# Kernel optimization log

Hardware: AMD Instinct MI355X
Metric: run time of the kernel (lower is better)

## Reference

```python
import jax, jax.numpy as jnp
import numpy as np

B, S, D = 1, 2048, 2048
H, KVH, HD = 32, 8, 64
FFN = 8192
N_EXPERTS, TOP_K = 32, 4
EPS = 1e-5
NEG = -1e9


def setup_inputs() -> dict:
    key = jax.random.key(0)
    ks = jax.random.split(key, 24)
    s = 0.02
    inp = {}
    inp['hidden_states'] = jax.random.normal(ks[0], (B, S, D), jnp.float32)
    # RoPE tables: cos/sin of shape [B, S, HD]
    inv_freq = 1.0 / (10000.0 ** (np.arange(0, HD, 2, dtype=np.float32) / HD))
    t = np.arange(S, dtype=np.float32)
    freqs = np.outer(t, inv_freq)                      # [S, HD/2]
    emb = np.concatenate([freqs, freqs], axis=-1)      # [S, HD]
    inp['cos'] = jnp.asarray(np.cos(emb))[None].repeat(B, axis=0)
    inp['sin'] = jnp.asarray(np.sin(emb))[None].repeat(B, axis=0)
    # additive causal mask [B, 1, S, S]
    causal = jnp.where(jnp.tril(jnp.ones((S, S), bool)), 0.0, NEG).astype(jnp.float32)
    inp['attention_mask'] = jnp.broadcast_to(causal[None, None], (B, 1, S, S))
    # attention params
    inp['wq'] = jax.random.normal(ks[1], (H * HD, D), jnp.float32) * s
    inp['bq'] = jnp.zeros((H * HD,), jnp.float32)
    inp['wk'] = jax.random.normal(ks[2], (KVH * HD, D), jnp.float32) * s
    inp['bk'] = jnp.zeros((KVH * HD,), jnp.float32)
    inp['wv'] = jax.random.normal(ks[3], (KVH * HD, D), jnp.float32) * s
    inp['bv'] = jnp.zeros((KVH * HD,), jnp.float32)
    inp['wo'] = jax.random.normal(ks[4], (D, H * HD), jnp.float32) * s
    inp['bo'] = jnp.zeros((D,), jnp.float32)
    # norms
    inp['ln1_w'] = jnp.ones((D,), jnp.float32)
    inp['ln2_w'] = jnp.ones((D,), jnp.float32)
    # MoE gate + shared expert MLP
    inp['gate_w'] = jax.random.normal(ks[5], (N_EXPERTS, D), jnp.float32) * s
    inp['gate_b'] = jnp.zeros((N_EXPERTS,), jnp.float32)
    inp['w1'] = jax.random.normal(ks[6], (FFN, D), jnp.float32) * s
    inp['b1'] = jnp.zeros((FFN,), jnp.float32)
    inp['w2'] = jax.random.normal(ks[7], (D, FFN), jnp.float32) * s
    inp['b2'] = jnp.zeros((D,), jnp.float32)
    inp['w3'] = jax.random.normal(ks[8], (FFN, D), jnp.float32) * s
    inp['b3'] = jnp.zeros((FFN,), jnp.float32)
    return inp


def _rms_norm(x, w, eps=EPS):
    x32 = x.astype(jnp.float32)
    var = jnp.mean(x32 * x32, axis=-1, keepdims=True)
    return (w * (x32 * jax.lax.rsqrt(var + eps))).astype(x.dtype)


def _rotate_half(x):
    x1, x2 = jnp.split(x, 2, axis=-1)
    return jnp.concatenate([-x2, x1], axis=-1)


def _decoder_layer(hidden_states, cos, sin, attention_mask,
                   wq, bq, wk, bk, wv, bv, wo, bo, ln1_w, ln2_w,
                   gate_w, gate_b, w1, b1, w2, b2, w3, b3):
    residual = hidden_states
    x = _rms_norm(hidden_states, ln1_w)

    # projections -> [B, heads, S, HD]
    q = (x @ wq.T + bq).reshape(B, S, H, HD).transpose(0, 2, 1, 3)
    k = (x @ wk.T + bk).reshape(B, S, KVH, HD).transpose(0, 2, 1, 3)
    v = (x @ wv.T + bv).reshape(B, S, KVH, HD).transpose(0, 2, 1, 3)

    # RoPE (cos/sin unsqueezed on head dim)
    c, s_ = cos[:, None], sin[:, None]
    q = q * c + _rotate_half(q) * s_
    k = k * c + _rotate_half(k) * s_

    # GQA: repeat kv heads
    n_rep = H // KVH
    k = jnp.repeat(k, n_rep, axis=1)
    v = jnp.repeat(v, n_rep, axis=1)

    scaling = HD ** -0.5
    scores = jnp.einsum('bhqd,bhkd->bhqk', q, k) * scaling + attention_mask
    probs = jax.nn.softmax(scores.astype(jnp.float32), axis=-1).astype(q.dtype)
    attn = jnp.einsum('bhqk,bhkd->bhqd', probs, v)
    attn = attn.transpose(0, 2, 1, 3).reshape(B, S, H * HD)
    attn = attn @ wo.T + bo

    hidden_states = residual + attn
    residual = hidden_states
    x = _rms_norm(hidden_states, ln2_w)

    # MoE block (as written in source: router computed, but ALL tokens go
    # through one shared expert MLP; routing weights unused in output)
    flat = x.reshape(-1, D)
    router_logits = flat @ gate_w.T + gate_b                     # [B*S, E]
    rw = jax.nn.softmax(router_logits.astype(jnp.float32), axis=-1)
    rw_top, sel = jax.lax.top_k(rw, TOP_K)                       # computed, unused
    del rw_top, sel

    h1 = flat @ w1.T + b1
    h3 = flat @ w3.T + b3
    mlp = (jax.nn.silu(h1) * h3) @ w2.T + b2
    hidden_states = residual + mlp.reshape(B, S, D)
    return hidden_states


def reference(hidden_states, cos, sin, attention_mask,
              wq, bq, wk, bk, wv, bv, wo, bo, ln1_w, ln2_w,
              gate_w, gate_b, w1, b1, w2, b2, w3, b3):
    return _decoder_layer(hidden_states, cos, sin, attention_mask,
                          wq, bq, wk, bk, wv, bv, wo, bo, ln1_w, ln2_w,
                          gate_w, gate_b, w1, b1, w2, b2, w3, b3)
```

## Files before the change

kernel.cpp:

```cpp
#include <hip/hip_runtime.h>

#define S_LEN 2048
#define DMODEL 2048
#define NH 32
#define NKV 8
#define HD 64
#define FFN_DIM 8192

typedef __attribute__((ext_vector_type(4))) float f32x4;
typedef __attribute__((ext_vector_type(16))) float f32x16;
typedef __attribute__((ext_vector_type(8))) short bf16x8;

#define MFMA(a, b, c) __builtin_amdgcn_mfma_f32_16x16x32_bf16(a, b, c, 0, 0, 0)
#define MFMA32(a, b, c) __builtin_amdgcn_mfma_f32_32x32x16_bf16(a, b, c, 0, 0, 0)

__device__ __forceinline__ ushort f2bf(float f) {
  unsigned u = __float_as_uint(f);
  unsigned r = (u + 0x7fffu + ((u >> 16) & 1u)) >> 16;
  return (ushort)r;
}
__device__ __forceinline__ float bf2f(ushort s) {
  return __uint_as_float(((unsigned)s) << 16);
}
__device__ __forceinline__ unsigned cvtpk(float a, float b) {
  unsigned r;
  asm("v_cvt_pk_bf16_f32 %0, %1, %2" : "=v"(r) : "v"(a), "v"(b));
  return r;
}

__device__ __forceinline__ void gload16(const void* g, void* l) {
  __builtin_amdgcn_global_load_lds(
      (const __attribute__((address_space(1))) void*)g,
      (__attribute__((address_space(3))) void*)l, 16, 0, 0);
}

__global__ __launch_bounds__(256) void cvt_k(const float* __restrict__ in,
                                             ushort* __restrict__ out) {
  int i = blockIdx.x * 256 + threadIdx.x;
  f32x4 a = ((const f32x4*)in)[i * 2];
  f32x4 b = ((const f32x4*)in)[i * 2 + 1];
  bf16x8 r;
#pragma unroll
  for (int j = 0; j < 4; j++) r[j] = (short)f2bf(a[j]);
#pragma unroll
  for (int j = 0; j < 4; j++) r[4 + j] = (short)f2bf(b[j]);
  ((bf16x8*)out)[i] = r;
}

__global__ __launch_bounds__(256) void cvt_qkv_k(const float* __restrict__ wq,
                                                 const float* __restrict__ wk,
                                                 const float* __restrict__ wv,
                                                 ushort* __restrict__ dst) {
  int row = blockIdx.x;
  const float* src;
  if (row < 2048) src = wq + (size_t)row * DMODEL;
  else if (row < 2560) src = wk + (size_t)(row - 2048) * DMODEL;
  else src = wv + (size_t)(row - 2560) * DMODEL;
  int i = threadIdx.x * 8;
  f32x4 a = *(const f32x4*)(src + i);
  f32x4 b = *(const f32x4*)(src + i + 4);
  bf16x8 r;
#pragma unroll
  for (int j = 0; j < 4; j++) r[j] = (short)f2bf(a[j]);
#pragma unroll
  for (int j = 0; j < 4; j++) r[4 + j] = (short)f2bf(b[j]);
  *(bf16x8*)(dst + (size_t)row * DMODEL + i) = r;
}

__global__ __launch_bounds__(256) void cvt_w13_k(const float* __restrict__ w1,
                                                 const float* __restrict__ w3,
                                                 ushort* __restrict__ dst) {
  int r = blockIdx.x;
  int nb = r >> 8, i5 = r & 255;
  int wn = i5 >> 6, nf = (i5 >> 4) & 3, e = i5 & 15;
  int L = nb * 128 + wn * 32 + (nf >> 1) * 16 + e;
  const float* src = ((nf & 1) ? w3 : w1) + (size_t)L * DMODEL;
  int i = threadIdx.x * 8;
  f32x4 a = *(const f32x4*)(src + i);
  f32x4 b = *(const f32x4*)(src + i + 4);
  bf16x8 rr;
#pragma unroll
  for (int j = 0; j < 4; j++) rr[j] = (short)f2bf(a[j]);
#pragma unroll
  for (int j = 0; j < 4; j++) rr[4 + j] = (short)f2bf(b[j]);
  *(bf16x8*)(dst + (size_t)r * DMODEL + i) = rr;
}

__global__ __launch_bounds__(256) void bias3_k(const float* __restrict__ a,
                                               const float* __restrict__ b,
                                               const float* __restrict__ c,
                                               float* __restrict__ out) {
  int i = blockIdx.x * 256 + threadIdx.x;
  float v;
  if (i < 2048) v = a[i];
  else if (i < 2560) v = b[i - 2048];
  else v = c[i - 2560];
  out[i] = v;
}

__global__ __launch_bounds__(256) void rmsnorm_k(const float* __restrict__ in,
                                                 const float* __restrict__ w,
                                                 ushort* __restrict__ out) {
  const int row = blockIdx.x;
  const int tid = threadIdx.x;
  const float* x = in + (size_t)row * DMODEL;
  f32x4 v0 = *(const f32x4*)(x + tid * 8);
  f32x4 v1 = *(const f32x4*)(x + tid * 8 + 4);
  float ss = v0[0] * v0[0] + v0[1] * v0[1] + v0[2] * v0[2] + v0[3] * v0[3] +
             v1[0] * v1[0] + v1[1] * v1[1] + v1[2] * v1[2] + v1[3] * v1[3];
#pragma unroll
  for (int off = 32; off; off >>= 1) ss += __shfl_xor(ss, off, 64);
  __shared__ float red[4];
  if ((tid & 63) == 0) red[tid >> 6] = ss;
  __syncthreads();
  float tot = red[0] + red[1] + red[2] + red[3];
  float inv = rsqrtf(tot * (1.f / DMODEL) + 1e-5f);
#pragma unroll
  for (int i = 0; i < 8; i++) {
    int c = tid * 8 + i;
    float val = (i < 4) ? v0[i] : v1[i - 4];
    out[(size_t)row * DMODEL + c] = f2bf(w[c] * val * inv);
  }
}

enum { EPI_PART = 0, EPI_SILU2 = 1 };

#define QUAD(AS, BS, MROW, NCOL)                                     \
  _Pragma("unroll") for (int kk_ = 0; kk_ < 2; kk_++)                \
  _Pragma("unroll") for (int mf_ = 0; mf_ < 4; mf_++)                \
  _Pragma("unroll") for (int nf_ = 0; nf_ < 2; nf_++)                \
      acc[(MROW) + mf_][(NCOL) + nf_] =                              \
          MFMA(AS[2 * mf_ + kk_], BS[2 * nf_ + kk_],                 \
               acc[(MROW) + mf_][(NCOL) + nf_]);

#define PHASE_MID                                    \
  __builtin_amdgcn_sched_barrier(0);                 \
  __builtin_amdgcn_s_barrier();                      \
  asm volatile("s_waitcnt lgkmcnt(0)" ::: "memory"); \
  __builtin_amdgcn_sched_barrier(0);                 \
  __builtin_amdgcn_s_setprio(1);

#define PHASE_CLOSE                                  \
  __builtin_amdgcn_s_setprio(0);                     \
  __builtin_amdgcn_sched_barrier(0);                 \
  __builtin_amdgcn_s_barrier();

#define RD_A(PA0, PA1, J0)                           \
  _Pragma("unroll") for (int j_ = 0; j_ < 4; j_++) { \
    A_[2 * j_] = *(const bf16x8*)((PA0) + ((J0) + j_) * 1024);     \
    A_[2 * j_ + 1] = *(const bf16x8*)((PA1) + ((J0) + j_) * 1024); \
  }
#define RD_B(DST, PB0, PB1, J0)                      \
  _Pragma("unroll") for (int n_ = 0; n_ < 2; n_++) { \
    DST[2 * n_] = *(const bf16x8*)((PB0) + ((J0) + n_) * 1024);     \
    DST[2 * n_ + 1] = *(const bf16x8*)((PB1) + ((J0) + n_) * 1024); \
  }

template <int EPI>
__global__ __launch_bounds__(512, 2) void gemm256(
    const ushort* __restrict__ A, int lda, const ushort* __restrict__ B,
    int ldb, const float* __restrict__ b1v, const float* __restrict__ b3v,
    ushort* __restrict__ outb, int ldc, int K, int kspan, long long opart) {
  __shared__ __align__(16) ushort lds[65536];
  const int tid = threadIdx.x;
  const int l = tid & 63, w = tid >> 6;
  const int g = l >> 4, r16 = l & 15;
  const int wm = w >> 2, wn = w & 3;

  int nwg = gridDim.x * gridDim.y;
  int bid = blockIdx.y * gridDim.x + blockIdx.x;
  bid = (bid & 7) * (nwg >> 3) + (bid >> 3);
  const int m0 = (bid % gridDim.x) * 256;
  const int n0 = (bid / gridDim.x) * 256;
  const int z = blockIdx.z;

  const ushort* Ag = A + (size_t)z * kspan + (size_t)m0 * lda;
  const ushort* Bg = B + (size_t)z * kspan + (size_t)n0 * ldb;
  ushort* outbz = outb + (size_t)z * opart;

  const int NT = K >> 6, NI = NT >> 1;

  const int stgRow = w * 8 + (l >> 3);
  const int stgCol = ((l & 7) ^ (l >> 3)) * 8;

  const int xa = (r16 & 7) << 4;
  const int c0 = ((g * 16) ^ xa) >> 1;
  const int c1 = c0 ^ 32;
  const int aslot = wm ? 24576 : 8192;
  const int bslot = ((wn >> 1) ? 16384 : 0) + (wn & 1) * 4096;
  const ushort* pA0b0 = lds + aslot + r16 * 64 + c0;
  const ushort* pA1b0 = lds + aslot + r16 * 64 + c1;
  const ushort* pA0b1 = pA0b0 + 32768;
  const ushort* pA1b1 = pA1b0 + 32768;
  const ushort* pB0b0 = lds + bslot + r16 * 64 + c0;
  const ushort* pB1b0 = lds + bslot + r16 * 64 + c1;
  const ushort* pB0b1 = pB0b0 + 32768;
  const ushort* pB1b1 = pB1b0 + 32768;

  f32x4 acc[8][4];
#pragma unroll
  for (int i = 0; i < 8; i++)
#pragma unroll
    for (int j = 0; j < 4; j++) acc[i][j] = (f32x4){0, 0, 0, 0};

  auto stageA = [&](int slot, int tile, int hf) {
    ushort* dst = lds + ((tile & 1) * 32768 + slot * 8192 + w * 512);
    const ushort* src =
        Ag + (size_t)(hf * 128 + stgRow) * lda + tile * 64 + stgCol;
    gload16(src, dst);
    gload16(src + (size_t)64 * lda, dst + 4096);
  };
  auto stageB = [&](int slot, int tile, int hf) {
    ushort* dst = lds + ((tile & 1) * 32768 + slot * 8192 + w * 512);
    const ushort* src =
        Bg + (size_t)(hf * 128 + stgRow) * ldb + tile * 64 + stgCol;
    gload16(src, dst);
    gload16(src + (size_t)64 * ldb, dst + 4096);
  };

  stageB(0, 0, 0);
  stageB(2, 0, 1);
  stageA(1, 0, 0);
  stageA(3, 0, 1);
  stageB(0, 1, 0);
  stageB(2, 1, 1);
  asm volatile("s_waitcnt vmcnt(4)" ::: "memory");
  __builtin_amdgcn_s_barrier();

  bf16x8 A_[8], Blo[4], Bhi[4];

  for (int i = 0; i < NI; ++i) {
    const int ta = 2 * i, tb = 2 * i + 1;
    const bool st = (ta + 2 < NT);
    RD_A(pA0b0, pA1b0, 0);
    RD_B(Blo, pB0b0, pB1b0, 0);
    stageA(1, tb, 0);
    asm volatile("s_waitcnt lgkmcnt(8)" ::: "memory");
    PHASE_MID; QUAD(A_, Blo, 0, 0); PHASE_CLOSE;
    RD_B(Bhi, pB0b0, pB1b0, 2);
    stageA(3, tb, 1);
    PHASE_MID; QUAD(A_, Bhi, 0, 2); PHASE_CLOSE;
    RD_A(pA0b0, pA1b0, 4);
    if (st) stageB(0, ta + 2, 0);
    PHASE_MID; QUAD(A_, Bhi, 4, 2); PHASE_CLOSE;
    if (st) stageB(2, ta + 2, 1);
    PHASE_MID; QUAD(A_, Blo, 4, 0);
    __builtin_amdgcn_s_setprio(0);
    __builtin_amdgcn_sched_barrier(0);
    if (st) {
      asm volatile("s_waitcnt vmcnt(4)" ::: "memory");
    } else {
      asm volatile("s_waitcnt vmcnt(0)" ::: "memory");
    }
    __builtin_amdgcn_s_barrier();
    RD_A(pA0b1, pA1b1, 0);
    RD_B(Blo, pB0b1, pB1b1, 0);
    if (st) stageA(1, ta + 2, 0);
    asm volatile("s_waitcnt lgkmcnt(8)" ::: "memory");
    PHASE_MID; QUAD(A_, Blo, 0, 0); PHASE_CLOSE;
    RD_B(Bhi, pB0b1, pB1b1, 2);
    if (st) stageA(3, ta + 2, 1);
    PHASE_MID; QUAD(A_, Bhi, 0, 2); PHASE_CLOSE;
    RD_A(pA0b1, pA1b1, 4);
    if (st) stageB(0, tb + 2, 0);
    PHASE_MID; QUAD(A_, Bhi, 4, 2); PHASE_CLOSE;
    if (st) stageB(2, tb + 2, 1);
    PHASE_MID; QUAD(A_, Blo, 4, 0);
    __builtin_amdgcn_s_setprio(0);
    __builtin_amdgcn_sched_barrier(0);
    asm volatile("s_waitcnt vmcnt(4)" ::: "memory");
    __builtin_amdgcn_s_barrier();
  }

  if constexpr (EPI == EPI_PART) {
#pragma unroll
    for (int mf = 0; mf < 8; mf++)
#pragma unroll
      for (int nf = 0; nf < 4; nf++) {
        const int n = n0 + wn * 64 + nf * 16 + r16;
#pragma unroll
        for (int reg = 0; reg < 4; reg++) {
          const int m = m0 + wm * 128 + mf * 16 + g * 4 + reg;
          outbz[(size_t)m * ldc + n] = f2bf(acc[mf][nf][reg]);
        }
      }
  } else {
#pragma unroll
    for (int mf = 0; mf < 8; mf++)
#pragma unroll
      for (int p = 0; p < 2; p++) {
        const int L = (n0 >> 1) + wn * 32 + p * 16 + r16;
        const float bb1 = b1v[L], bb3 = b3v[L];
#pragma unroll
        for (int reg = 0; reg < 4; reg++) {
          const int m = m0 + wm * 128 + mf * 16 + g * 4 + reg;
          float h1 = acc[mf][2 * p][reg] + bb1;
          float h3 = acc[mf][2 * p + 1][reg] + bb3;
          float sv = h1 / (1.f + __expf(-h1));
          outbz[(size_t)m * ldc + L] = f2bf(sv * h3);
        }
      }
  }
}

__global__ __launch_bounds__(384) void reduceQ_rope_k(
    const ushort* __restrict__ part, const float* __restrict__ bias,
    const float* __restrict__ cs, const float* __restrict__ sn,
    ushort* __restrict__ qkv) {
  __shared__ float row[3072];
  const int r = blockIdx.x;
  const int col = threadIdx.x * 8;
  const long long ps = (long long)S_LEN * 3072;
  float s[8];
#pragma unroll
  for (int j = 0; j < 8; j++) s[j] = bias[col + j];
#pragma unroll
  for (int z = 0; z < 2; z++) {
    bf16x8 v = *(const bf16x8*)(part + z * ps + (size_t)r * 3072 + col);
#pragma unroll
    for (int j = 0; j < 8; j++) s[j] += bf2f((ushort)v[j]);
  }
#pragma unroll
  for (int j = 0; j < 8; j++) row[col + j] = s[j];
  __syncthreads();
  ushort o[8];
  if (col < 2560) {
    const float* c = cs + r * HD + (col & 63);
    const float* si = sn + r * HD + (col & 63);
    const float sgn = (col & 32) ? 1.f : -1.f;
    const int pc = col ^ 32;
#pragma unroll
    for (int j = 0; j < 8; j++)
      o[j] = f2bf(s[j] * c[j] + sgn * row[pc + j] * si[j]);
  } else {
#pragma unroll
    for (int j = 0; j < 8; j++) o[j] = f2bf(s[j]);
  }
  bf16x8 rr;
#pragma unroll
  for (int j = 0; j < 8; j++) rr[j] = (short)o[j];
  *(bf16x8*)(qkv + (size_t)r * 3072 + col) = rr;
}

__global__ __launch_bounds__(256) void reduceO_rms_k(
    const ushort* __restrict__ part, const float* __restrict__ bias,
    const float* __restrict__ resid, const float* __restrict__ lnw,
    float* __restrict__ outf, ushort* __restrict__ x2) {
  const int r = blockIdx.x;
  const int tid = threadIdx.x;
  const int col = tid * 8;
  const long long ps = (long long)S_LEN * DMODEL;
  float s[8];
#pragma unroll
  for (int j = 0; j < 8; j++) s[j] = bias[col + j] + resid[(size_t)r * DMODEL + col + j];
#pragma unroll
  for (int z = 0; z < 4; z++) {
    bf16x8 v = *(const bf16x8*)(part + z * ps + (size_t)r * DMODEL + col);
#pragma unroll
    for (int j = 0; j < 8; j++) s[j] += bf2f((ushort)v[j]);
  }
  float ss = 0.f;
#pragma unroll
  for (int j = 0; j < 8; j++) ss += s[j] * s[j];
#pragma unroll
  for (int off = 32; off; off >>= 1) ss += __shfl_xor(ss, off, 64);
  __shared__ float red[4];
  if ((tid & 63) == 0) red[tid >> 6] = ss;
  f32x4 o0, o1;
#pragma unroll
  for (int j = 0; j < 4; j++) { o0[j] = s[j]; o1[j] = s[4 + j]; }
  *(f32x4*)(outf + (size_t)r * DMODEL + col) = o0;
  *(f32x4*)(outf + (size_t)r * DMODEL + col + 4) = o1;
  __syncthreads();
  float tot = red[0] + red[1] + red[2] + red[3];
  float inv = rsqrtf(tot * (1.f / DMODEL) + 1e-5f);
  bf16x8 rr;
#pragma unroll
  for (int j = 0; j < 8; j++) rr[j] = (short)f2bf(lnw[col + j] * s[j] * inv);
  *(bf16x8*)(x2 + (size_t)r * DMODEL + col) = rr;
}

__global__ __launch_bounds__(256) void reduceW_k(
    const ushort* __restrict__ part, const float* __restrict__ bias,
    float* __restrict__ out) {
  long long i = (long long)(blockIdx.x * 256 + threadIdx.x) * 8;
  int col = (int)(i % DMODEL);
  const long long ps = (long long)S_LEN * DMODEL;
  float s[8];
#pragma unroll
  for (int j = 0; j < 8; j++) s[j] = bias[col + j] + out[i + j];
#pragma unroll
  for (int z = 0; z < 4; z++) {
    bf16x8 v = *(const bf16x8*)(part + z * ps + i);
#pragma unroll
    for (int j = 0; j < 8; j++) s[j] += bf2f((ushort)v[j]);
  }
#pragma unroll
  for (int j = 0; j < 8; j++) out[i + j] = s[j];
}

__global__ __launch_bounds__(256, 3) void flash2_k(const ushort* __restrict__ qkv,
                                                   ushort* __restrict__ att) {
  const int bid = blockIdx.x;
  const int head = (bid >> 4) & 31;
  const int rmap = bid & 15;
  const int qb = (bid & 256) ? (15 - rmap) : rmap;
  const int kvh = head >> 2;
  const int tid = threadIdx.x;
  const int w = tid >> 6, l = tid & 63;
  const int h = l >> 5, q31 = l & 31;
  const int qw = qb * 128 + w * 32;
  const int qrow = qw + q31;

  __shared__ __align__(16) ushort lds[2][8192];

  bf16x8 qreg[4];
  {
    const ushort* qp = qkv + (size_t)qrow * 3072 + head * HD;
#pragma unroll
    for (int s = 0; s < 4; s++)
      qreg[s] = *(const bf16x8*)(qp + s * 16 + h * 8);
  }

  f32x16 oacc[2];
#pragma unroll
  for (int i = 0; i < 16; i++) { oacc[0][i] = 0.f; oacc[1][i] = 0.f; }
  float mreg = -1e30f, lsum = 0.f;

  const int nt = 2 * qb + 2;

  const int skv = tid >> 2;
  const int sch = (tid & 3) * 2;
  const int vkv = tid & 63;
  const int vd0 = (tid >> 6) * 16;

  const ushort* kg_base = qkv + DMODEL + kvh * HD;

  bf16x8 krA, krB, vrA, vrB;
  auto loadTile = [&](int jb) {
    const ushort* kg = kg_base + (size_t)jb * 64 * 3072;
    krA = *(const bf16x8*)(kg + (size_t)skv * 3072 + sch * 8);
    krB = *(const bf16x8*)(kg + (size_t)skv * 3072 + sch * 8 + 8);
    const ushort* vg = kg + 512;
    vrA = *(const bf16x8*)(vg + (size_t)vkv * 3072 + vd0);
    vrB = *(const bf16x8*)(vg + (size_t)vkv * 3072 + vd0 + 8);
  };
  auto writeTile = [&](int b) {
    ushort* kb = lds[b];
    *(bf16x8*)(kb + skv * 64 + ((sch ^ (skv & 7)) * 8)) = krA;
    *(bf16x8*)(kb + skv * 64 + (((sch + 1) ^ (skv & 7)) * 8)) = krB;
    ushort* vb = lds[b] + 4096;
#pragma unroll
    for (int i = 0; i < 8; i++) {
      int d = vd0 + i;
      vb[d * 64 + (((vkv >> 3) ^ (d & 7)) * 8) + (vkv & 7)] = (ushort)vrA[i];
    }
#pragma unroll
    for (int i = 0; i < 8; i++) {
      int d = vd0 + 8 + i;
      vb[d * 64 + (((vkv >> 3) ^ (d & 7)) * 8) + (vkv & 7)] = (ushort)vrB[i];
    }
  };

  loadTile(0);
  for (int jb = 0; jb < nt; ++jb) {
    const int b = jb & 1;
    writeTile(b);
    __syncthreads();
    if (jb + 1 < nt) loadTile(jb + 1);

    if (jb * 64 <= qw + 31) {
      const ushort* Kb = lds[b];
      const ushort* Vb = lds[b] + 4096;

      f32x16 sacc[2];
#pragma unroll
      for (int i = 0; i < 16; i++) { sacc[0][i] = 0.f; sacc[1][i] = 0.f; }
#pragma unroll
      for (int c = 0; c < 2; c++) {
        const int kvr = c * 32 + q31;
        const ushort* kp = Kb + kvr * 64;
        const int kx = kvr & 7;
#pragma unroll
        for (int s = 0; s < 4; s++) {
          bf16x8 kf = *(const bf16x8*)(kp + ((2 * s + h) ^ kx) * 8);
          sacc[c] = MFMA32(kf, qreg[s], sacc[c]);
        }
      }

      const bool diag = (jb * 64 + 63 > qw);
      if (diag) {
#pragma unroll
        for (int c = 0; c < 2; c++)
#pragma unroll
          for (int rg = 0; rg < 16; rg++) {
            int kvg = jb * 64 + c * 32 + (rg & 3) + 8 * (rg >> 2) + 4 * h;
            if (kvg > qrow) sacc[c][rg] = -1e30f;
          }
      }
      float tmax = sacc[0][0];
#pragma unroll
      for (int rg = 1; rg < 16; rg++) tmax = fmaxf(tmax, sacc[0][rg]);
#pragma unroll
      for (int rg = 0; rg < 16; rg++) tmax = fmaxf(tmax, sacc[1][rg]);
      tmax = fmaxf(tmax, __shfl_xor(tmax, 32));
      const float mn = fmaxf(mreg, tmax);
      const float resc = __expf((mreg - mn) * 0.125f);
      mreg = mn;
      float rsum = 0.f;
#pragma unroll
      for (int c = 0; c < 2; c++)
#pragma unroll
        for (int rg = 0; rg < 16; rg++) {
          float pv = __expf((sacc[c][rg] - mn) * 0.125f);
          sacc[c][rg] = pv;
          rsum += pv;
        }
      rsum += __shfl_xor(rsum, 32);
      lsum = lsum * resc + rsum;
      oacc[0] *= resc;
      oacc[1] *= resc;

      unsigned pw_[2][4][2];
#pragma unroll
      for (int c = 0; c < 2; c++)
#pragma unroll
        for (int rr = 0; rr < 4; rr++) {
          pw_[c][rr][0] = cvtpk(sacc[c][4 * rr + 0], sacc[c][4 * rr + 1]);
          pw_[c][rr][1] = cvtpk(sacc[c][4 * rr + 2], sacc[c][4 * rr + 3]);
        }

#pragma unroll
      for (int s = 0; s < 4; s++) {
        const int c = s >> 1, base = (s & 1) * 2;
        unsigned k0 = h ? pw_[c][base + 1][0] : pw_[c][base][0];
        unsigned k1 = h ? pw_[c][base + 1][1] : pw_[c][base][1];
        unsigned s0 = h ? pw_[c][base][0] : pw_[c][base + 1][0];
        unsigned s1 = h ? pw_[c][base][1] : pw_[c][base + 1][1];
        unsigned t0 = __shfl_xor(s0, 32);
        unsigned t1 = __shfl_xor(s1, 32);
        union { unsigned u[4]; bf16x8 v; } pf;
        pf.u[0] = h ? t0 : k0;
        pf.u[1] = h ? t1 : k1;
        pf.u[2] = h ? k0 : t0;
        pf.u[3] = h ? k1 : t1;
#pragma unroll
        for (int dt = 0; dt < 2; dt++) {
          const int d = dt * 32 + q31;
          bf16x8 vf =
              *(const bf16x8*)(Vb + d * 64 + ((2 * s + h) ^ (d & 7)) * 8);
          oacc[dt] = MFMA32(vf, pf.v, oacc[dt]);
        }
      }
    }
  }

  const float inv = 1.f / lsum;
  ushort* op = att + (size_t)qrow * DMODEL + head * HD;
#pragma unroll
  for (int dt = 0; dt < 2; dt++)
#pragma unroll
    for (int rr = 0; rr < 4; rr++) {
      const int d0 = dt * 32 + 8 * rr + 4 * h;
      unsigned lo = cvtpk(oacc[dt][4 * rr + 0] * inv, oacc[dt][4 * rr + 1] * inv);
      unsigned hi = cvtpk(oacc[dt][4 * rr + 2] * inv, oacc[dt][4 * rr + 3] * inv);
      uint2 v2;
      v2.x = lo;
      v2.y = hi;
      *(uint2*)(op + d0) = v2;
    }
}

extern "C" void kernel_launch(void* const* d_in, const int* in_sizes, int n_in,
                              void* d_out, int out_size, void* d_ws,
                              size_t ws_size, hipStream_t stream) {
  (void)in_sizes; (void)n_in; (void)out_size; (void)ws_size;
  const float* hidden = (const float*)d_in[0];
  const float* cosb = (const float*)d_in[1];
  const float* sinb = (const float*)d_in[2];
  const float* wq = (const float*)d_in[4];
  const float* bq = (const float*)d_in[5];
  const float* wk = (const float*)d_in[6];
  const float* bk = (const float*)d_in[7];
  const float* wv = (const float*)d_in[8];
  const float* bv = (const float*)d_in[9];
  const float* wo = (const float*)d_in[10];
  const float* bo = (const float*)d_in[11];
  const float* ln1 = (const float*)d_in[12];
  const float* ln2 = (const float*)d_in[13];
  const float* w1 = (const float*)d_in[16];
  const float* b1 = (const float*)d_in[17];
  const float* w2 = (const float*)d_in[18];
  const float* b2 = (const float*)d_in[19];
  const float* w3 = (const float*)d_in[20];
  const float* b3 = (const float*)d_in[21];
  float* out = (float*)d_out;

  char* ws = (char*)d_ws;
  ushort* x1 = (ushort*)ws;   ws += (size_t)S_LEN * DMODEL * 2;
  ushort* qkv = (ushort*)ws;  ws += (size_t)S_LEN * 3072 * 2;
  ushort* att = (ushort*)ws;  ws += (size_t)S_LEN * DMODEL * 2;
  ushort* x2 = (ushort*)ws;   ws += (size_t)S_LEN * DMODEL * 2;
  ushort* hbuf = (ushort*)ws; ws += (size_t)S_LEN * FFN_DIM * 2;
  ushort* wbuf = (ushort*)ws; ws += (size_t)2 * FFN_DIM * DMODEL * 2;
  float* bqkv = (float*)ws;   ws += 3072 * 4;

  ushort* partQ = att;
  ushort* partO = hbuf;
  ushort* partW = x1;

  rmsnorm_k<<<S_LEN, 256, 0, stream>>>(hidden, ln1, x1);

  cvt_qkv_k<<<3072, 256, 0, stream>>>(wq, wk, wv, wbuf);
  bias3_k<<<12, 256, 0, stream>>>(bq, bk, bv, bqkv);

  gemm256<EPI_PART><<<dim3(8, 12, 2), 512, 0, stream>>>(
      x1, DMODEL, wbuf, DMODEL, nullptr, nullptr, partQ, 3072, 1024, 1024,
      (long long)S_LEN * 3072);
  reduceQ_rope_k<<<S_LEN, 384, 0, stream>>>(partQ, bqkv, cosb, sinb, qkv);

  flash2_k<<<512, 256, 0, stream>>>(qkv, att);

  cvt_k<<<(2048 * 2048) / 2048, 256, 0, stream>>>(wo, wbuf);
  gemm256<EPI_PART><<<dim3(8, 8, 4), 512, 0, stream>>>(
      att, DMODEL, wbuf, DMODEL, nullptr, nullptr, partO, DMODEL, 512, 512,
      (long long)S_LEN * DMODEL);
  reduceO_rms_k<<<S_LEN, 256, 0, stream>>>(partO, bo, hidden, ln2, out, x2);

  cvt_w13_k<<<2 * FFN_DIM, 256, 0, stream>>>(w1, w3, wbuf);
  gemm256<EPI_SILU2><<<dim3(8, 64), 512, 0, stream>>>(
      x2, DMODEL, wbuf, DMODEL, b1, b3, hbuf, FFN_DIM, DMODEL, 0, 0);

  cvt_k<<<(DMODEL * FFN_DIM) / 2048, 256, 0, stream>>>(w2, wbuf);
  gemm256<EPI_PART><<<dim3(8, 8, 4), 512, 0, stream>>>(
      hbuf, FFN_DIM, wbuf, FFN_DIM, nullptr, nullptr, partW, DMODEL, 2048,
      2048, (long long)S_LEN * DMODEL);
  reduceW_k<<<(S_LEN * DMODEL) / 2048, 256, 0, stream>>>(partW, b2, out);
}
```

Baseline: 381.8 us.

## Overlap wo/w13/w2 weight conversion with flash attention via extra blocks

Adds 256 extra blocks to the flash-attention launch that convert the wo, w1/w3 and w2 weights to bf16 while the attention blocks run. The three separate conversion launches are then skipped, and each later GEMM reads its own pre-converted buffer. This needs a second workspace region, so the old path is kept as a fallback when the workspace is too small. The intent is to hide the memory-bound conversion behind the compute-bound attention, at the cost of the two sharing CUs and bandwidth.

Result: no change. 378.4 us (-0.9%).

```diff
diff --git a/kernel.cpp b/kernel.cpp
--- a/kernel.cpp
+++ b/kernel.cpp
@@ -32,6 +32,18 @@
   __builtin_amdgcn_global_load_lds(
       (const __attribute__((address_space(1))) void*)g,
       (__attribute__((address_space(3))) void*)l, 16, 0, 0);
+}
+
+__device__ __forceinline__ void cvt_row8(const float* src, ushort* dst,
+                                         int i) {
+  f32x4 a = *(const f32x4*)(src + i);
+  f32x4 b = *(const f32x4*)(src + i + 4);
+  bf16x8 r;
+#pragma unroll
+  for (int j = 0; j < 4; j++) r[j] = (short)f2bf(a[j]);
+#pragma unroll
+  for (int j = 0; j < 4; j++) r[4 + j] = (short)f2bf(b[j]);
+  *(bf16x8*)(dst + i) = r;
 }
 
 __global__ __launch_bounds__(256) void cvt_k(const float* __restrict__ in,
@@ -56,15 +68,7 @@
   if (row < 2048) src = wq + (size_t)row * DMODEL;
   else if (row < 2560) src = wk + (size_t)(row - 2048) * DMODEL;
   else src = wv + (size_t)(row - 2560) * DMODEL;
-  int i = threadIdx.x * 8;
-  f32x4 a = *(const f32x4*)(src + i);
-  f32x4 b = *(const f32x4*)(src + i + 4);
-  bf16x8 r;
-#pragma unroll
-  for (int j = 0; j < 4; j++) r[j] = (short)f2bf(a[j]);
-#pragma unroll
-  for (int j = 0; j < 4; j++) r[4 + j] = (short)f2bf(b[j]);
-  *(bf16x8*)(dst + (size_t)row * DMODEL + i) = r;
+  cvt_row8(src, dst + (size_t)row * DMODEL, threadIdx.x * 8);
 }
 
 __global__ __launch_bounds__(256) void cvt_w13_k(const float* __restrict__ w1,
@@ -75,15 +79,7 @@
   int wn = i5 >> 6, nf = (i5 >> 4) & 3, e = i5 & 15;
   int L = nb * 128 + wn * 32 + (nf >> 1) * 16 + e;
   const float* src = ((nf & 1) ? w3 : w1) + (size_t)L * DMODEL;
-  int i = threadIdx.x * 8;
-  f32x4 a = *(const f32x4*)(src + i);
-  f32x4 b = *(const f32x4*)(src + i + 4);
-  bf16x8 rr;
-#pragma unroll
-  for (int j = 0; j < 4; j++) rr[j] = (short)f2bf(a[j]);
-#pragma unroll
-  for (int j = 0; j < 4; j++) rr[4 + j] = (short)f2bf(b[j]);
-  *(bf16x8*)(dst + (size_t)r * DMODEL + i) = rr;
+  cvt_row8(src, dst + (size_t)r * DMODEL, threadIdx.x * 8);
 }
 
 __global__ __launch_bounds__(256) void bias3_k(const float* __restrict__ a,
@@ -399,8 +395,37 @@
   for (int j = 0; j < 8; j++) out[i + j] = s[j];
 }
 
-__global__ __launch_bounds__(256, 3) void flash2_k(const ushort* __restrict__ qkv,
-                                                   ushort* __restrict__ att) {
+__global__ __launch_bounds__(256, 3) void flash2_k(
+    const ushort* __restrict__ qkv, ushort* __restrict__ att, int nFlash,
+    int nCvtTasks, const float* __restrict__ wo, const float* __restrict__ w1,
+    const float* __restrict__ w3, const float* __restrict__ w2s,
+    ushort* __restrict__ cwA, ushort* __restrict__ cwB) {
+  if ((int)blockIdx.x >= nFlash) {
+    const int cb = blockIdx.x - nFlash;
+    const int NC = gridDim.x - nFlash;
+    const int i = threadIdx.x * 8;
+    for (int t = cb; t < nCvtTasks; t += NC) {
+      const float* src;
+      ushort* dst;
+      if (t < 2048) {
+        src = wo + (size_t)t * DMODEL;
+        dst = cwB + (size_t)t * DMODEL;
+      } else if (t < 18432) {
+        int r = t - 2048;
+        int nb = r >> 8, i5 = r & 255;
+        int wn = i5 >> 6, nf = (i5 >> 4) & 3, e = i5 & 15;
+        int L = nb * 128 + wn * 32 + (nf >> 1) * 16 + e;
+        src = ((nf & 1) ? w3 : w1) + (size_t)L * DMODEL;
+        dst = cwA + (size_t)r * DMODEL;
+      } else {
+        int r = t - 18432;
+        src = w2s + (size_t)r * 2048;
+        dst = cwB + (size_t)2048 * DMODEL + (size_t)r * 2048;
+      }
+      cvt_row8(src, dst, i);
+    }
+    return;
+  }
   const int bid = blockIdx.x;
   const int head = (bid >> 4) & 31;
   const int rmap = bid & 15;
@@ -574,7 +599,7 @@
 extern "C" void kernel_launch(void* const* d_in, const int* in_sizes, int n_in,
                               void* d_out, int out_size, void* d_ws,
                               size_t ws_size, hipStream_t stream) {
-  (void)in_sizes; (void)n_in; (void)out_size; (void)ws_size;
+  (void)in_sizes; (void)n_in; (void)out_size;
   const float* hidden = (const float*)d_in[0];
   const float* cosb = (const float*)d_in[1];
   const float* sinb = (const float*)d_in[2];
@@ -596,14 +621,18 @@
   const float* b3 = (const float*)d_in[21];
   float* out = (float*)d_out;
 
-  char* ws = (char*)d_ws;
+  char* base = (char*)d_ws;
+  char* ws = base;
   ushort* x1 = (ushort*)ws;   ws += (size_t)S_LEN * DMODEL * 2;
   ushort* qkv = (ushort*)ws;  ws += (size_t)S_LEN * 3072 * 2;
   ushort* att = (ushort*)ws;  ws += (size_t)S_LEN * DMODEL * 2;
   ushort* x2 = (ushort*)ws;   ws += (size_t)S_LEN * DMODEL * 2;
   ushort* hbuf = (ushort*)ws; ws += (size_t)S_LEN * FFN_DIM * 2;
-  ushort* wbuf = (ushort*)ws; ws += (size_t)2 * FFN_DIM * DMODEL * 2;
-  float* bqkv = (float*)ws;   ws += 3072 * 4;
+  ushort* cwA = (ushort*)ws;  ws += (size_t)2 * FFN_DIM * DMODEL * 2;
+  float* bqkv = (float*)ws;   ws += 4096 * 4;
+  ushort* cwB = (ushort*)ws;
+  const size_t cwB_bytes = (size_t)(2048 + 8192) * DMODEL * 2;
+  const bool bigws = ((size_t)(ws - base) + cwB_bytes) <= ws_size;
 
   ushort* partQ = att;
   ushort* partO = hbuf;
@@ -611,29 +640,42 @@
 
   rmsnorm_k<<<S_LEN, 256, 0, stream>>>(hidden, ln1, x1);
 
-  cvt_qkv_k<<<3072, 256, 0, stream>>>(wq, wk, wv, wbuf);
+  cvt_qkv_k<<<3072, 256, 0, stream>>>(wq, wk, wv, cwA);
   bias3_k<<<12, 256, 0, stream>>>(bq, bk, bv, bqkv);
 
   gemm256<EPI_PART><<<dim3(8, 12, 2), 512, 0, stream>>>(
-      x1, DMODEL, wbuf, DMODEL, nullptr, nullptr, partQ, 3072, 1024, 1024,
+      x1, DMODEL, cwA, DMODEL, nullptr, nullptr, partQ, 3072, 1024, 1024,
       (long long)S_LEN * 3072);
   reduceQ_rope_k<<<S_LEN, 384, 0, stream>>>(partQ, bqkv, cosb, sinb, qkv);
 
-  flash2_k<<<512, 256, 0, stream>>>(qkv, att);
-
-  cvt_k<<<(2048 * 2048) / 2048, 256, 0, stream>>>(wo, wbuf);
+  const ushort *Bo, *B13, *B2;
+  if (bigws) {
+    flash2_k<<<512 + 256, 256, 0, stream>>>(qkv, att, 512, 26624, wo, w1, w3,
+                                            w2, cwA, cwB);
+    Bo = cwB;
+    B13 = cwA;
+    B2 = cwB + (size_t)2048 * DMODEL;
+  } else {
+    flash2_k<<<512, 256, 0, stream>>>(qkv, att, 512, 0, wo, w1, w3, w2, cwA,
+                                      cwA);
+    Bo = cwA;
+    B13 = cwA;
+    B2 = cwA;
+  }
+
+  if (!bigws) cvt_k<<<(2048 * 2048) / 2048, 256, 0, stream>>>(wo, (ushort*)Bo);
   gemm256<EPI_PART><<<dim3(8, 8, 4), 512, 0, stream>>>(
-      att, DMODEL, wbuf, DMODEL, nullptr, nullptr, partO, DMODEL, 512, 512,
+      att, DMODEL, Bo, DMODEL, nullptr, nullptr, partO, DMODEL, 512, 512,
       (long long)S_LEN * DMODEL);
   reduceO_rms_k<<<S_LEN, 256, 0, stream>>>(partO, bo, hidden, ln2, out, x2);
 
-  cvt_w13_k<<<2 * FFN_DIM, 256, 0, stream>>>(w1, w3, wbuf);
+  if (!bigws) cvt_w13_k<<<2 * FFN_DIM, 256, 0, stream>>>(w1, w3, (ushort*)B13);
   gemm256<EPI_SILU2><<<dim3(8, 64), 512, 0, stream>>>(
-      x2, DMODEL, wbuf, DMODEL, b1, b3, hbuf, FFN_DIM, DMODEL, 0, 0);
-
-  cvt_k<<<(DMODEL * FFN_DIM) / 2048, 256, 0, stream>>>(w2, wbuf);
+      x2, DMODEL, B13, DMODEL, b1, b3, hbuf, FFN_DIM, DMODEL, 0, 0);
+
+  if (!bigws) cvt_k<<<(DMODEL * FFN_DIM) / 2048, 256, 0, stream>>>(w2, (ushort*)B2);
   gemm256<EPI_PART><<<dim3(8, 8, 4), 512, 0, stream>>>(
-      hbuf, FFN_DIM, wbuf, FFN_DIM, nullptr, nullptr, partW, DMODEL, 2048,
-      2048, (long long)S_LEN * DMODEL);
+      hbuf, FFN_DIM, B2, FFN_DIM, nullptr, nullptr, partW, DMODEL, 2048, 2048,
+      (long long)S_LEN * DMODEL);
   reduceW_k<<<(S_LEN * DMODEL) / 2048, 256, 0, stream>>>(partW, b2, out);
 }
```
